# Kernel tuning notes

Hardware: AMD Instinct MI355X
Metric: run time of the kernel (lower is better)

## Reference

```python
import jax, jax.numpy as jnp
import numpy as np

B, L, D, H = 2, 2048, 1024, 16
HD = D // H
KW = 4  # conv kernel width


def layernorm(x, g, b, eps=1e-5):
    m = jnp.mean(x, axis=-1, keepdims=True)
    v = jnp.var(x, axis=-1, keepdims=True)
    return (x - m) / jnp.sqrt(v + eps) * g + b


def causal_conv(x, w, b):
    # torch Conv1d(k=4, padding=3, groups=D) then truncate to L => causal depthwise conv
    # out[t] = sum_j w[:, j] * x[t - 3 + j] + b
    xp = jnp.pad(x, ((0, 0), (KW - 1, 0), (0, 0)))
    Lx = x.shape[1]
    out = b
    for j in range(KW):
        out = out + xp[:, j:j + Lx, :] * w[:, j]
    return out


def setup_inputs() -> dict:
    key = jax.random.key(0)
    ks = jax.random.split(key, 16)
    r = lambda i, shape, s=0.02: jax.random.normal(ks[i], shape, jnp.float32) * s
    return dict(
        x=r(0, (B, L, D), 1.0),
        Wqkv=r(1, (D, 3 * D)), Wout=r(2, (D, D)),
        Wgate=r(3, (D, D)), bgate=jnp.zeros((D,), jnp.float32),
        fn_g=jnp.ones((D,), jnp.float32), fn_b=jnp.zeros((D,), jnp.float32),
        dn_g=jnp.ones((D,), jnp.float32), dn_b=jnp.zeros((D,), jnp.float32),
        dWq=r(4, (D, D)), dWk=r(5, (D, D)), dWv=r(6, (D, D)), dWo=r(7, (D, D)),
        Wbeta=r(8, (D, H)), bbeta=jnp.zeros((H,), jnp.float32),
        cq_w=r(9, (D, KW), 0.1), cq_b=jnp.zeros((D,), jnp.float32),
        ck_w=r(10, (D, KW), 0.1), ck_b=jnp.zeros((D,), jnp.float32),
        ln_g=jnp.ones((D,), jnp.float32), ln_b=jnp.zeros((D,), jnp.float32),
    )


def _delta_scan(q, k, v, beta):
    # q,k,v: (B,L,H,HD) ; beta: (B,L,H)
    Bx = q.shape[0]
    S0 = jnp.zeros((Bx, H, HD, HD), q.dtype)
    z0 = jnp.zeros((Bx, H, HD), q.dtype)

    def step(carry, inp):
        S, z = carry
        q_t, k_t, v_t, b_t = inp  # (B,H,HD) x3, (B,H)
        y = jnp.einsum('bhij,bhj->bhi', S, q_t)
        denom = jnp.einsum('bhi,bhi->bh', z, q_t)[..., None] + 1e-6
        y = y / denom
        old = jnp.einsum('bhij,bhj->bhi', S, k_t)
        delta = v_t - old
        S = S + b_t[..., None, None] * jnp.einsum('bhi,bhj->bhij', delta, k_t)
        z = z + b_t[..., None] * k_t
        return (S, z), y

    xs = (jnp.moveaxis(q, 1, 0), jnp.moveaxis(k, 1, 0),
          jnp.moveaxis(v, 1, 0), jnp.moveaxis(beta, 1, 0))
    (S, z), ys = jax.lax.scan(step, (S0, z0), xs)
    return jnp.moveaxis(ys, 0, 1), S, z  # (B,L,H,HD)


def _forward(x, Wqkv, Wout, Wgate, bgate, fn_g, fn_b, dn_g, dn_b,
             dWq, dWk, dWv, dWo, Wbeta, bbeta, cq_w, cq_b, ck_w, ck_b, ln_g, ln_b):
    Bx, Lx, Dx = x.shape
    # ---- flash (full causal, L<=2048 branch) ----
    qkv = (x @ Wqkv).reshape(Bx, Lx, 3, H, HD)
    q = jnp.moveaxis(qkv[:, :, 0], 1, 2)  # (B,H,L,HD)
    k = jnp.moveaxis(qkv[:, :, 1], 1, 2)
    v = jnp.moveaxis(qkv[:, :, 2], 1, 2)
    scale = HD ** -0.5
    scores = jnp.einsum('bhqd,bhkd->bhqk', q, k) * scale
    causal = jnp.tril(jnp.ones((Lx, Lx), bool))
    scores = jnp.where(causal, scores, -jnp.inf)
    attn = jax.nn.softmax(scores, axis=-1)
    flash = jnp.einsum('bhqk,bhkd->bhqd', attn, v)
    flash = jnp.moveaxis(flash, 1, 2).reshape(Bx, Lx, Dx) @ Wout
    flash = layernorm(flash, fn_g, fn_b)
    # ---- delta branch ----
    dq = causal_conv(x @ dWq, cq_w, cq_b).reshape(Bx, Lx, H, HD)
    dk = causal_conv(x @ dWk, ck_w, ck_b).reshape(Bx, Lx, H, HD)
    dv = (x @ dWv).reshape(Bx, Lx, H, HD)
    dk = dk / jnp.maximum(jnp.linalg.norm(dk, axis=-1, keepdims=True), 1e-12)
    beta = jax.nn.sigmoid(x @ Wbeta + bbeta)  # (B,L,H)
    ys, S, z = _delta_scan(dq, dk, dv, beta)
    delta_out = layernorm(ys.reshape(Bx, Lx, Dx) @ dWo, ln_g, ln_b)  # DeltaAttention layer_norm
    delta_out = layernorm(delta_out, dn_g, dn_b)  # hybrid delta_norm
    # ---- gate ----
    gate = jax.nn.sigmoid(x @ Wgate + bgate)
    out = gate * flash + (1.0 - gate) * delta_out
    return out, S, z


def reference(x, Wqkv, Wout, Wgate, bgate, fn_g, fn_b, dn_g, dn_b,
              dWq, dWk, dWv, dWo, Wbeta, bbeta, cq_w, cq_b, ck_w, ck_b, ln_g, ln_b):
    return _forward(x, Wqkv, Wout, Wgate, bgate, fn_g, fn_b, dn_g, dn_b,
                    dWq, dWk, dWv, dWo, Wbeta, bbeta, cq_w, cq_b, ck_w, ck_b, ln_g, ln_b)
```

## Files before the change

### kernel.cpp

```cpp
#include <hip/hip_runtime.h>
#include <hip/hip_bf16.h>

constexpr int B_ = 2, L_ = 2048, D_ = 1024, H_ = 16;

using bf16x8 = __attribute__((ext_vector_type(8))) short;
using f32x4  = __attribute__((ext_vector_type(4))) float;

__device__ __forceinline__ short f2b(float f) {
  union { float f; unsigned int u; } v; v.f = f;
  unsigned int r = (v.u + 0x7FFFu + ((v.u >> 16) & 1u)) >> 16;
  return (short)r;
}
__device__ __forceinline__ float b2f(unsigned short h) {
  union { unsigned int u; float f; } v; v.u = ((unsigned int)h) << 16; return v.f;
}
__device__ __forceinline__ void split2(float x, float y, unsigned int& h, unsigned int& l) {
  unsigned short hx = (unsigned short)f2b(x), hy = (unsigned short)f2b(y);
  h = (unsigned int)hx | ((unsigned int)hy << 16);
  unsigned short lx = (unsigned short)f2b(x - b2f(hx)), ly = (unsigned short)f2b(y - b2f(hy));
  l = (unsigned int)lx | ((unsigned int)ly << 16);
}
__device__ __forceinline__ float dot4(float4 a, float4 b) {
  return a.x * b.x + a.y * b.y + a.z * b.z + a.w * b.w;
}

__global__ __launch_bounds__(256) void tcast(const float* __restrict__ W, short* __restrict__ Wt,
                                             int N, int K) {
  __shared__ float T[64][65];
  int n0 = blockIdx.x * 64, k0 = blockIdx.y * 64;
  int tid = threadIdx.x;
#pragma unroll
  for (int i = 0; i < 16; ++i) {
    int idx = i * 256 + tid;
    int r = idx >> 6, c = idx & 63;
    T[r][c] = W[(size_t)(k0 + r) * N + n0 + c];
  }
  __syncthreads();
#pragma unroll
  for (int i = 0; i < 16; ++i) {
    int idx = i * 256 + tid;
    int rr = idx >> 6, cc = idx & 63;
    Wt[(size_t)(n0 + rr) * K + k0 + cc] = f2b(T[cc][rr]);
  }
}

__global__ __launch_bounds__(256) void tcast2(const float* __restrict__ W1, const float* __restrict__ W2,
                                              short* __restrict__ Wt1, short* __restrict__ Wt2) {
  __shared__ float T[64][65];
  const float* W = blockIdx.z ? W2 : W1;
  short* Wt = blockIdx.z ? Wt2 : Wt1;
  int n0 = blockIdx.x * 64, k0 = blockIdx.y * 64;
  int tid = threadIdx.x;
#pragma unroll
  for (int i = 0; i < 16; ++i) {
    int idx = i * 256 + tid;
    int r = idx >> 6, c = idx & 63;
    T[r][c] = W[(size_t)(k0 + r) * 1024 + n0 + c];
  }
  __syncthreads();
#pragma unroll
  for (int i = 0; i < 16; ++i) {
    int idx = i * 256 + tid;
    int rr = idx >> 6, cc = idx & 63;
    Wt[(size_t)(n0 + rr) * 1024 + k0 + cc] = f2b(T[cc][rr]);
  }
}

__global__ __launch_bounds__(256) void tcast_split2(const float* __restrict__ W1, const float* __restrict__ W2,
                                                    short* __restrict__ Wh1, short* __restrict__ Wl1,
                                                    short* __restrict__ Wh2, short* __restrict__ Wl2) {
  __shared__ float T[64][65];
  const float* W = blockIdx.z ? W2 : W1;
  short* Wh = blockIdx.z ? Wh2 : Wh1;
  short* Wl = blockIdx.z ? Wl2 : Wl1;
  int n0 = blockIdx.x * 64, k0 = blockIdx.y * 64;
  int tid = threadIdx.x;
#pragma unroll
  for (int i = 0; i < 16; ++i) {
    int idx = i * 256 + tid;
    int r = idx >> 6, c = idx & 63;
    T[r][c] = W[(size_t)(k0 + r) * 1024 + n0 + c];
  }
  __syncthreads();
#pragma unroll
  for (int i = 0; i < 16; ++i) {
    int idx = i * 256 + tid;
    int rr = idx >> 6, cc = idx & 63;
    float w = T[cc][rr];
    short h = f2b(w);
    short l = f2b(w - b2f((unsigned short)h));
    size_t o = (size_t)(n0 + rr) * 1024 + k0 + cc;
    Wh[o] = h;
    Wl[o] = l;
  }
}

template <int BN, typename CT>
__device__ __forceinline__ void gemm_bt_body(const float* __restrict__ A, const short* __restrict__ Wt,
                                             CT* __restrict__ C, int N, int K, int bx, int by) {
  constexpr int MT = (BN == 128) ? 4 : 2;
  constexpr int NT = 4;
  __shared__ __align__(16) short As[128 * 32];
  __shared__ __align__(16) short Bs[BN * 32];
  int tid = threadIdx.x;
  int wave = tid >> 6, lane = tid & 63, quad = lane >> 4, l15 = lane & 15;
  int m0 = by * 128, n0 = bx * BN;
  int wm = (BN == 128) ? (wave >> 1) * 64 : wave * 32;
  int wn = (BN == 128) ? (wave & 1) * 64 : 0;
  f32x4 acc[MT][NT];
#pragma unroll
  for (int mt = 0; mt < MT; ++mt)
#pragma unroll
    for (int nt = 0; nt < NT; ++nt) acc[mt][nt] = (f32x4){0.f, 0.f, 0.f, 0.f};

  for (int k0 = 0; k0 < K; k0 += 32) {
    __syncthreads();
#pragma unroll
    for (int i = 0; i < 2; ++i) {
      int chunk = i * 256 + tid;
      int m = chunk >> 2, kc = (chunk & 3) * 8;
      const float* ap = A + (size_t)(m0 + m) * K + k0 + kc;
      float4 a0 = *(const float4*)ap;
      float4 a1 = *(const float4*)(ap + 4);
      __hip_bfloat162 c0 = __float22bfloat162_rn(make_float2(a0.x, a0.y));
      __hip_bfloat162 c1 = __float22bfloat162_rn(make_float2(a0.z, a0.w));
      __hip_bfloat162 c2 = __float22bfloat162_rn(make_float2(a1.x, a1.y));
      __hip_bfloat162 c3 = __float22bfloat162_rn(make_float2(a1.z, a1.w));
      uint4 u;
      u.x = *(unsigned int*)&c0; u.y = *(unsigned int*)&c1;
      u.z = *(unsigned int*)&c2; u.w = *(unsigned int*)&c3;
      *(uint4*)&As[m * 32 + kc] = u;
    }
#pragma unroll
    for (int i = 0; i < BN * 4 / 256; ++i) {
      int chunk = i * 256 + tid;
      int n = chunk >> 2, kc = (chunk & 3) * 8;
      uint4 w = *(const uint4*)(Wt + (size_t)(n0 + n) * K + k0 + kc);
      *(uint4*)&Bs[n * 32 + kc] = w;
    }
    __syncthreads();
    bf16x8 af[MT], bf[NT];
#pragma unroll
    for (int mt = 0; mt < MT; ++mt) af[mt] = *(bf16x8*)&As[(wm + mt * 16 + l15) * 32 + quad * 8];
#pragma unroll
    for (int nt = 0; nt < NT; ++nt) bf[nt] = *(bf16x8*)&Bs[(wn + nt * 16 + l15) * 32 + quad * 8];
#pragma unroll
    for (int mt = 0; mt < MT; ++mt)
#pragma unroll
      for (int nt = 0; nt < NT; ++nt)
        acc[mt][nt] = __builtin_amdgcn_mfma_f32_16x16x32_bf16(af[mt], bf[nt], acc[mt][nt], 0, 0, 0);
  }
#pragma unroll
  for (int mt = 0; mt < MT; ++mt)
#pragma unroll
    for (int nt = 0; nt < NT; ++nt)
#pragma unroll
      for (int r = 0; r < 4; ++r) {
        size_t idx = (size_t)(m0 + wm + mt * 16 + quad * 4 + r) * N + n0 + wn + nt * 16 + l15;
        if constexpr (sizeof(CT) == 2) C[idx] = f2b(acc[mt][nt][r]);
        else C[idx] = acc[mt][nt][r];
      }
}

template <int BN>
__global__ __launch_bounds__(256) void gemm_bt(const float* __restrict__ A, const short* __restrict__ Wt,
                                               float* __restrict__ C, int N, int K) {
  gemm_bt_body<BN, float>(A, Wt, C, N, K, blockIdx.x, blockIdx.y);
}

__global__ __launch_bounds__(256) void gemm_bt_h(const float* __restrict__ A, const short* __restrict__ Wt,
                                                 short* __restrict__ C, int N, int K) {
  gemm_bt_body<128, short>(A, Wt, C, N, K, blockIdx.x, blockIdx.y);
}

__global__ __launch_bounds__(256) void gemm_bt2(const float* __restrict__ A, const short* __restrict__ Wt1,
                                                const short* __restrict__ Wt2, float* __restrict__ C1,
                                                float* __restrict__ C2) {
  gemm_bt_body<64, float>(A, blockIdx.z ? Wt2 : Wt1, blockIdx.z ? C2 : C1, 1024, 1024,
                          blockIdx.x, blockIdx.y);
}

__global__ __launch_bounds__(256) void gemm_bt_split2(const float* __restrict__ A,
                                                      const short* __restrict__ Wh1, const short* __restrict__ Wl1,
                                                      const short* __restrict__ Wh2, const short* __restrict__ Wl2,
                                                      float* __restrict__ C1, float* __restrict__ C2) {
  constexpr int K = 1024, N = 1024;
  const short* Wh = blockIdx.z ? Wh2 : Wh1;
  const short* Wl = blockIdx.z ? Wl2 : Wl1;
  float* C = blockIdx.z ? C2 : C1;
  __shared__ __align__(16) short Ash[128 * 32];
  __shared__ __align__(16) short Asl[128 * 32];
  __shared__ __align__(16) short Bsh[64 * 32];
  __shared__ __align__(16) short Bsl[64 * 32];
  int tid = threadIdx.x;
  int wave = tid >> 6, lane = tid & 63, quad = lane >> 4, l15 = lane & 15;
  int m0 = blockIdx.y * 128, n0 = blockIdx.x * 64;
  int wm = wave * 32;
  f32x4 acc[2][4];
#pragma unroll
  for (int mt = 0; mt < 2; ++mt)
#pragma unroll
    for (int nt = 0; nt < 4; ++nt) acc[mt][nt] = (f32x4){0.f, 0.f, 0.f, 0.f};

  for (int k0 = 0; k0 < K; k0 += 32) {
    __syncthreads();
#pragma unroll
    for (int i = 0; i < 2; ++i) {
      int chunk = i * 256 + tid;
      int m = chunk >> 2, kc = (chunk & 3) * 8;
      const float* ap = A + (size_t)(m0 + m) * K + k0 + kc;
      float4 a0 = *(const float4*)ap;
      float4 a1 = *(const float4*)(ap + 4);
      uint4 uh, ul;
      split2(a0.x, a0.y, uh.x, ul.x);
      split2(a0.z, a0.w, uh.y, ul.y);
      split2(a1.x, a1.y, uh.z, ul.z);
      split2(a1.z, a1.w, uh.w, ul.w);
      *(uint4*)&Ash[m * 32 + kc] = uh;
      *(uint4*)&Asl[m * 32 + kc] = ul;
    }
    {
      int n = tid >> 2, kc = (tid & 3) * 8;
      size_t off = (size_t)(n0 + n) * K + k0 + kc;
      *(uint4*)&Bsh[n * 32 + kc] = *(const uint4*)(Wh + off);
      *(uint4*)&Bsl[n * 32 + kc] = *(const uint4*)(Wl + off);
    }
    __syncthreads();
    bf16x8 ah[2], al[2], bh[4], bl[4];
#pragma unroll
    for (int mt = 0; mt < 2; ++mt) {
      ah[mt] = *(bf16x8*)&Ash[(wm + mt * 16 + l15) * 32 + quad * 8];
      al[mt] = *(bf16x8*)&Asl[(wm + mt * 16 + l15) * 32 + quad * 8];
    }
#pragma unroll
    for (int nt = 0; nt < 4; ++nt) {
      bh[nt] = *(bf16x8*)&Bsh[(nt * 16 + l15) * 32 + quad * 8];
      bl[nt] = *(bf16x8*)&Bsl[(nt * 16 + l15) * 32 + quad * 8];
    }
#pragma unroll
    for (int mt = 0; mt < 2; ++mt)
#pragma unroll
      for (int nt = 0; nt < 4; ++nt) {
        f32x4 a = acc[mt][nt];
        a = __builtin_amdgcn_mfma_f32_16x16x32_bf16(al[mt], bh[nt], a, 0, 0, 0);
        a = __builtin_amdgcn_mfma_f32_16x16x32_bf16(ah[mt], bl[nt], a, 0, 0, 0);
        a = __builtin_amdgcn_mfma_f32_16x16x32_bf16(ah[mt], bh[nt], a, 0, 0, 0);
        acc[mt][nt] = a;
      }
  }
#pragma unroll
  for (int mt = 0; mt < 2; ++mt)
#pragma unroll
    for (int nt = 0; nt < 4; ++nt)
#pragma unroll
      for (int r = 0; r < 4; ++r) {
        size_t idx = (size_t)(m0 + wm + mt * 16 + quad * 4 + r) * N + n0 + nt * 16 + l15;
        C[idx] = acc[mt][nt][r];
      }
}

__global__ __launch_bounds__(256) void attn_mfma(const short* __restrict__ qkv, float* __restrict__ outp) {
  __shared__ __align__(16) short Kl[64 * 64];
  __shared__ __align__(16) short Vt[64 * 64];
  __shared__ __align__(16) short Pl[64 * 64];
  int qb = 31 - blockIdx.x, h = blockIdx.y, b = blockIdx.z;
  int tid = threadIdx.x;
  int wave = tid >> 6, lane = tid & 63;
  int quad = lane >> 4, l15 = lane & 15;
  int qrow = qb * 64 + wave * 16 + l15;
  bf16x8 qf[2];
  {
    const short* qbase = qkv + (size_t)(b * L_ + qrow) * 3072 + h * 64;
#pragma unroll
    for (int s = 0; s < 2; ++s) qf[s] = *(const bf16x8*)(qbase + s * 32 + quad * 8);
  }
  f32x4 Of[4];
  float mrow[4], lrow[4], alpha[4];
#pragma unroll
  for (int dt = 0; dt < 4; ++dt) Of[dt] = (f32x4){0.f, 0.f, 0.f, 0.f};
#pragma unroll
  for (int r = 0; r < 4; ++r) { mrow[r] = -1e30f; lrow[r] = 0.f; }

  for (int kt = 0; kt <= qb; ++kt) {
    __syncthreads();
#pragma unroll
    for (int it = 0; it < 2; ++it) {
      int e8 = tid + it * 256;
      int key = e8 >> 3, g = e8 & 7;
      const short* src = qkv + ((size_t)((b * L_ + kt * 64 + key) * 3) + 1) * 1024 + h * 64 + g * 8;
      *(bf16x8*)&Kl[key * 64 + ((g ^ (key & 7)) << 3)] = *(const bf16x8*)src;
    }
    {
      int key4 = tid >> 4;
      int d4 = tid & 15;
      const short* vsrc = qkv + ((size_t)((b * L_ + kt * 64 + key4 * 4) * 3) + 2) * 1024 + h * 64 + d4 * 4;
      short4 v0 = *(const short4*)vsrc;
      short4 v1 = *(const short4*)(vsrc + 3072);
      short4 v2 = *(const short4*)(vsrc + 6144);
      short4 v3 = *(const short4*)(vsrc + 9216);
      short vr0[4] = {v0.x, v0.y, v0.z, v0.w};
      short vr1[4] = {v1.x, v1.y, v1.z, v1.w};
      short vr2[4] = {v2.x, v2.y, v2.z, v2.w};
      short vr3[4] = {v3.x, v3.y, v3.z, v3.w};
      int kg = key4 >> 1, k7b = (key4 & 1) * 4;
#pragma unroll
      for (int jj = 0; jj < 4; ++jj) {
        int d = d4 * 4 + jj;
        short4 sv;
        sv.x = vr0[jj]; sv.y = vr1[jj]; sv.z = vr2[jj]; sv.w = vr3[jj];
        *(short4*)&Vt[d * 64 + ((kg ^ (d & 7)) << 3) + k7b] = sv;
      }
    }
    __syncthreads();
    f32x4 sc[4];
#pragma unroll
    for (int nt = 0; nt < 4; ++nt) sc[nt] = (f32x4){0.f, 0.f, 0.f, 0.f};
#pragma unroll
    for (int s = 0; s < 2; ++s) {
#pragma unroll
      for (int nt = 0; nt < 4; ++nt) {
        int key = nt * 16 + l15;
        bf16x8 kf = *(bf16x8*)&Kl[key * 64 + (((4 * s + quad) ^ (key & 7)) << 3)];
        sc[nt] = __builtin_amdgcn_mfma_f32_16x16x32_bf16(qf[s], kf, sc[nt], 0, 0, 0);
      }
    }
    bool diag = (kt == qb);
#pragma unroll
    for (int r = 0; r < 4; ++r) {
      float sv[4];
#pragma unroll
      for (int nt = 0; nt < 4; ++nt) {
        float v = sc[nt][r] * 0.125f;
        if (diag && (nt * 16 + l15 > wave * 16 + quad * 4 + r)) v = -1e30f;
        sv[nt] = v;
      }
      float mx = fmaxf(fmaxf(sv[0], sv[1]), fmaxf(sv[2], sv[3]));
      mx = fmaxf(mx, __shfl_xor(mx, 1));
      mx = fmaxf(mx, __shfl_xor(mx, 2));
      mx = fmaxf(mx, __shfl_xor(mx, 4));
      mx = fmaxf(mx, __shfl_xor(mx, 8));
      float mnew = fmaxf(mrow[r], mx);
      float al = __expf(mrow[r] - mnew);
      mrow[r] = mnew;
      alpha[r] = al;
      int prow = wave * 16 + quad * 4 + r;
      int r7 = prow & 7;
      float ps = 0.f;
#pragma unroll
      for (int nt = 0; nt < 4; ++nt) {
        float p = __expf(sv[nt] - mnew);
        ps += p;
        Pl[prow * 64 + ((((nt << 1) + (l15 >> 3)) ^ r7) << 3) + (l15 & 7)] = f2b(p);
      }
      ps += __shfl_xor(ps, 1);
      ps += __shfl_xor(ps, 2);
      ps += __shfl_xor(ps, 4);
      ps += __shfl_xor(ps, 8);
      lrow[r] = lrow[r] * al + ps;
    }
#pragma unroll
    for (int dt = 0; dt < 4; ++dt)
#pragma unroll
      for (int r = 0; r < 4; ++r) Of[dt][r] *= alpha[r];
#pragma unroll
    for (int s = 0; s < 2; ++s) {
      bf16x8 pf = *(bf16x8*)&Pl[(wave * 16 + l15) * 64 + (((4 * s + quad) ^ (l15 & 7)) << 3)];
#pragma unroll
      for (int dt = 0; dt < 4; ++dt) {
        int d = dt * 16 + l15;
        bf16x8 vf = *(bf16x8*)&Vt[d * 64 + (((4 * s + quad) ^ (d & 7)) << 3)];
        Of[dt] = __builtin_amdgcn_mfma_f32_16x16x32_bf16(pf, vf, Of[dt], 0, 0, 0);
      }
    }
  }
#pragma unroll
  for (int r = 0; r < 4; ++r) alpha[r] = 1.f / lrow[r];
  int orow = qb * 64 + wave * 16 + quad * 4;
#pragma unroll
  for (int dt = 0; dt < 4; ++dt)
#pragma unroll
    for (int r = 0; r < 4; ++r)
      outp[(size_t)(b * L_ + orow + r) * 1024 + h * 64 + dt * 16 + l15] = Of[dt][r] * alpha[r];
}

__global__ __launch_bounds__(256) void ln_kernel(float* __restrict__ X, const float* __restrict__ g,
                                                 const float* __restrict__ bb) {
  int row = blockIdx.x, tid = threadIdx.x;
  float* xr = X + (size_t)row * D_;
  float v[4], s = 0.f, ss = 0.f;
#pragma unroll
  for (int i = 0; i < 4; ++i) { v[i] = xr[tid + i * 256]; s += v[i]; ss += v[i] * v[i]; }
#pragma unroll
  for (int off = 32; off; off >>= 1) { s += __shfl_xor(s, off); ss += __shfl_xor(ss, off); }
  __shared__ float rs[4], rss[4];
  if ((tid & 63) == 0) { rs[tid >> 6] = s; rss[tid >> 6] = ss; }
  __syncthreads();
  float S = rs[0] + rs[1] + rs[2] + rs[3];
  float SS = rss[0] + rss[1] + rss[2] + rss[3];
  float mean = S * (1.f / 1024.f);
  float var = SS * (1.f / 1024.f) - mean * mean;
  float inv = rsqrtf(var + 1e-5f);
#pragma unroll
  for (int i = 0; i < 4; ++i) {
    int c = tid + i * 256;
    xr[c] = (v[i] - mean) * inv * g[c] + bb[c];
  }
}

__global__ __launch_bounds__(256) void ln2mix_kernel(const float* __restrict__ X,
                                                     const float* __restrict__ g1, const float* __restrict__ b1,
                                                     const float* __restrict__ g2, const float* __restrict__ b2,
                                                     const float* __restrict__ gpre, const float* __restrict__ bgate,
                                                     const float* __restrict__ fo, float* __restrict__ outp) {
  int row = blockIdx.x, tid = threadIdx.x;
  const float* xr = X + (size_t)row * D_;
  __shared__ float rs[4], rss[4];
  float v[4], s = 0.f, ss = 0.f;
#pragma unroll
  for (int i = 0; i < 4; ++i) { v[i] = xr[tid + i * 256]; s += v[i]; ss += v[i] * v[i]; }
#pragma unroll
  for (int off = 32; off; off >>= 1) { s += __shfl_xor(s, off); ss += __shfl_xor(ss, off); }
  if ((tid & 63) == 0) { rs[tid >> 6] = s; rss[tid >> 6] = ss; }
  __syncthreads();
  float S = rs[0] + rs[1] + rs[2] + rs[3];
  float SS = rss[0] + rss[1] + rss[2] + rss[3];
  float mean = S * (1.f / 1024.f);
  float var = SS * (1.f / 1024.f) - mean * mean;
  float inv = rsqrtf(var + 1e-5f);
  s = 0.f; ss = 0.f;
#pragma unroll
  for (int i = 0; i < 4; ++i) {
    int c = tid + i * 256;
    v[i] = (v[i] - mean) * inv * g1[c] + b1[c];
    s += v[i]; ss += v[i] * v[i];
  }
#pragma unroll
  for (int off = 32; off; off >>= 1) { s += __shfl_xor(s, off); ss += __shfl_xor(ss, off); }
  __syncthreads();
  if ((tid & 63) == 0) { rs[tid >> 6] = s; rss[tid >> 6] = ss; }
  __syncthreads();
  S = rs[0] + rs[1] + rs[2] + rs[3];
  SS = rss[0] + rss[1] + rss[2] + rss[3];
  mean = S * (1.f / 1024.f);
  var = SS * (1.f / 1024.f) - mean * mean;
  inv = rsqrtf(var + 1e-5f);
#pragma unroll
  for (int i = 0; i < 4; ++i) {
    int c = tid + i * 256;
    size_t idx = (size_t)row * D_ + c;
    float w = (v[i] - mean) * inv * g2[c] + b2[c];
    float gg = 1.f / (1.f + __expf(-(gpre[idx] + bgate[c])));
    outp[idx] = gg * fo[idx] + (1.f - gg) * w;
  }
}

__global__ __launch_bounds__(256) void convnorm_kernel(const float* __restrict__ qin, const float* __restrict__ kin,
                                                       const float* __restrict__ qw, const float* __restrict__ qb,
                                                       const float* __restrict__ kw, const float* __restrict__ kb,
                                                       float* __restrict__ qout, float* __restrict__ kout) {
  int path = blockIdx.y;
  int row = blockIdx.x * 4 + (threadIdx.x >> 6);
  int lane = threadIdx.x & 63;
  int bl = row >> 4, h = row & 15;
  int t = bl & (L_ - 1);
  int d = h * 64 + lane;
  size_t idx = (size_t)bl * D_ + d;
  const float* xin = path ? kin : qin;
  const float* w = path ? kw : qw;
  const float* bias = path ? kb : qb;
  float acc = bias[d];
#pragma unroll
  for (int j = 0; j < 4; ++j) {
    int tt = t - 3 + j;
    if (tt >= 0) acc += w[d * 4 + j] * xin[idx + (size_t)(j - 3) * D_];
  }
  if (path) {
    float n2 = acc * acc;
#pragma unroll
    for (int off = 32; off; off >>= 1) n2 += __shfl_xor(n2, off);
    acc = acc / fmaxf(sqrtf(n2), 1e-12f);
    kout[idx] = acc;
  } else {
    qout[idx] = acc;
  }
}

__global__ __launch_bounds__(256) void beta_kernel(const float* __restrict__ xf, const float* __restrict__ Wb,
                                                   const float* __restrict__ bb, float* __restrict__ beta) {
  int row = blockIdx.x, tid = threadIdx.x;
  int h = tid & 15, seg = tid >> 4;
  const float* xr = xf + (size_t)row * D_ + seg * 64;
  const float* wp = Wb + (seg * 64) * H_ + h;
  float p = 0.f;
  for (int k = 0; k < 64; ++k) p += xr[k] * wp[k * H_];
  __shared__ float red[16][17];
  red[seg][h] = p;
  __syncthreads();
  if (tid < 16) {
    float s = bb[tid];
#pragma unroll
    for (int s2 = 0; s2 < 16; ++s2) s += red[s2][tid];
    beta[(size_t)row * H_ + tid] = 1.f / (1.f + __expf(-s));
  }
}

__global__ __launch_bounds__(256) void prep_kernel(const float* __restrict__ dq, const float* __restrict__ dk,
                                                   const float* __restrict__ beta,
                                                   float* __restrict__ Minv_g, float* __restrict__ Bq_g) {
  __shared__ __align__(16) float Kl[32 * 68];
  __shared__ __align__(16) float Ql[32 * 68];
  __shared__ __align__(16) float Ml[32 * 36];
  __shared__ __align__(16) float Xl[32 * 36];
  __shared__ __align__(16) float bl[32];
  int c = blockIdx.x, bh = blockIdx.y;
  int b = bh >> 4, h = bh & 15;
  int t0 = c * 32;
  int tid = threadIdx.x;
#pragma unroll
  for (int rep = 0; rep < 2; ++rep) {
    int id = tid * 2 + rep;
    int r = id >> 4, j4 = id & 15;
    size_t gi = (size_t)(b * L_ + t0 + r) * 1024 + h * 64 + j4 * 4;
    *(float4*)&Kl[r * 68 + j4 * 4] = *(const float4*)&dk[gi];
    *(float4*)&Ql[r * 68 + j4 * 4] = *(const float4*)&dq[gi];
  }
  if (tid < 32) bl[tid] = beta[(size_t)(b * L_ + t0 + tid) * 16 + h];
  __syncthreads();
  int t = tid >> 3, s0 = (tid & 7) * 4;
  float accA[4] = {0.f, 0.f, 0.f, 0.f}, accB[4] = {0.f, 0.f, 0.f, 0.f};
#pragma unroll
  for (int k4 = 0; k4 < 16; ++k4) {
    float4 kt = *(float4*)&Kl[t * 68 + k4 * 4];
    float4 qt = *(float4*)&Ql[t * 68 + k4 * 4];
#pragma unroll
    for (int j = 0; j < 4; ++j) {
      float4 ks = *(float4*)&Kl[(s0 + j) * 68 + k4 * 4];
      accA[j] += dot4(kt, ks);
      accB[j] += dot4(qt, ks);
    }
  }
  float4 bq;
  float* bqp = (float*)&bq;
#pragma unroll
  for (int j = 0; j < 4; ++j) {
    int s = s0 + j;
    Ml[t * 36 + s] = (s < t) ? bl[t] * accA[j] : ((s == t) ? 1.f : 0.f);
    bqp[j] = (s < t) ? accB[j] : 0.f;
  }
  size_t obase = ((size_t)(bh * 64 + c) * 32 + t) * 32 + s0;
  *(float4*)&Bq_g[obase] = bq;
  __syncthreads();
  if (tid < 32) {
    int col = tid;
    float xr[32];
#pragma unroll
    for (int tt = 0; tt < 32; ++tt) {
      float x = (tt == col) ? 1.f : 0.f;
#pragma unroll
      for (int s = 0; s < tt; ++s) x -= Ml[tt * 36 + s] * xr[s];
      xr[tt] = x;
      Xl[tt * 36 + col] = x;
    }
  }
  __syncthreads();
  float4 mv = make_float4(Xl[t * 36 + s0], Xl[t * 36 + s0 + 1], Xl[t * 36 + s0 + 2], Xl[t * 36 + s0 + 3]);
  *(float4*)&Minv_g[obase] = mv;
}

__global__ __launch_bounds__(256) void delta_kernel(const float* __restrict__ dq, const float* __restrict__ dk,
                                                    const float* __restrict__ dv, const float* __restrict__ beta,
                                                    const float* __restrict__ Minv_g, const float* __restrict__ Bq_g,
                                                    float* __restrict__ ys, float* __restrict__ outS,
                                                    float* __restrict__ outZ) {
  __shared__ __align__(16) float Kl[32 * 68];
  __shared__ __align__(16) float Ql[32 * 68];
  __shared__ __align__(16) float Vl[32 * 5];
  __shared__ __align__(16) float Mil[32 * 36];
  __shared__ __align__(16) float Bql[32 * 36];
  __shared__ __align__(16) float bl[32];
  __shared__ __align__(16) float S0l[4 * 68];
  __shared__ __align__(16) float Y0l[32 * 5];
  __shared__ __align__(16) float RtmpTl[4 * 36];
  __shared__ __align__(16) float RTl[4 * 36];
  __shared__ __align__(16) float z0l[68];
  __shared__ __align__(16) float qzl[32];
  __shared__ __align__(16) float denl[32];
  int bh = blockIdx.x & 31, grp = blockIdx.x >> 5;
  int b = bh >> 4, h = bh & 15;
  int i0 = grp * 4;
  int tid = threadIdx.x;
  int r = tid >> 3, j8 = (tid & 7) * 8, s4 = tid & 7;
  size_t kqbase = (size_t)(b * L_) * 1024 + h * 64;

  for (int e = tid; e < 4 * 68; e += 256) S0l[e] = 0.f;
  if (tid < 68) z0l[tid] = 0.f;

  float4 kA, kB, qA, qB, mr, br;
  float vr = 0.f, blr = 0.f;
  {
    const float* kp = dk + kqbase + (size_t)r * 1024 + j8;
    kA = ((const float4*)kp)[0]; kB = ((const float4*)kp)[1];
    const float* qp = dq + kqbase + (size_t)r * 1024 + j8;
    qA = ((const float4*)qp)[0]; qB = ((const float4*)qp)[1];
    size_t gb = ((size_t)(bh * 64) * 32 + r) * 32 + s4 * 4;
    mr = *(const float4*)&Minv_g[gb];
    br = *(const float4*)&Bq_g[gb];
    if (tid < 128) vr = dv[(size_t)(b * L_ + (tid >> 2)) * 1024 + h * 64 + i0 + (tid & 3)];
    if (tid < 32) blr = beta[(size_t)(b * L_ + tid) * 16 + h];
  }
  *(float4*)&Kl[r * 68 + j8] = kA; *(float4*)&Kl[r * 68 + j8 + 4] = kB;
  *(float4*)&Ql[r * 68 + j8] = qA; *(float4*)&Ql[r * 68 + j8 + 4] = qB;
  *(float4*)&Mil[r * 36 + s4 * 4] = mr;
  *(float4*)&Bql[r * 36 + s4 * 4] = br;
  if (tid < 128) Vl[(tid >> 2) * 5 + (tid & 3)] = vr;
  if (tid < 32) bl[tid] = blr;
  __syncthreads();

  for (int c = 0; c < 64; ++c) {
    int cn = (c + 1 < 64) ? c + 1 : 63;
    int t0n = cn * 32;
    {
      const float* kp = dk + kqbase + (size_t)(t0n + r) * 1024 + j8;
      kA = ((const float4*)kp)[0]; kB = ((const float4*)kp)[1];
      const float* qp = dq + kqbase + (size_t)(t0n + r) * 1024 + j8;
      qA = ((const float4*)qp)[0]; qB = ((const float4*)qp)[1];
      size_t gb = ((size_t)(bh * 64 + cn) * 32 + r) * 32 + s4 * 4;
      mr = *(const float4*)&Minv_g[gb];
      br = *(const float4*)&Bq_g[gb];
      if (tid < 128) vr = dv[(size_t)(b * L_ + t0n + (tid >> 2)) * 1024 + h * 64 + i0 + (tid & 3)];
      if (tid < 32) blr = beta[(size_t)(b * L_ + t0n + tid) * 16 + h];
    }
    int t0 = c * 32;
    {
      int jh = tid & 1;
      int i = (tid >> 1) & 3;
      int t = tid >> 3;
      float aK = 0.f, aY = 0.f;
#pragma unroll
      for (int jj = 0; jj < 8; ++jj) {
        int j4 = jh * 8 + jj;
        float4 k = *(float4*)&Kl[t * 68 + j4 * 4];
        float4 q = *(float4*)&Ql[t * 68 + j4 * 4];
        float4 s = *(float4*)&S0l[i * 68 + j4 * 4];
        aK += dot4(k, s);
        aY += dot4(q, s);
      }
      aK += __shfl_xor(aK, 1);
      aY += __shfl_xor(aY, 1);
      if (jh == 0) {
        float be = bl[t];
        RtmpTl[i * 36 + t] = be * (Vl[t * 5 + i] - aK);
        Y0l[t * 5 + i] = aY;
      }
      if (tid < 32) {
        float a = 0.f;
#pragma unroll
        for (int j4 = 0; j4 < 16; ++j4) {
          float4 q = *(float4*)&Ql[tid * 68 + j4 * 4];
          float4 z = *(float4*)&z0l[j4 * 4];
          a += dot4(q, z);
        }
        qzl[tid] = a;
      }
    }
    __syncthreads();
    {
      if (tid < 128) {
        int t = tid >> 2, i = tid & 3;
        float acc = 0.f;
#pragma unroll
        for (int s4i = 0; s4i < 8; ++s4i) {
          float4 m = *(float4*)&Mil[t * 36 + s4i * 4];
          float4 rt = *(float4*)&RtmpTl[i * 36 + s4i * 4];
          acc += dot4(m, rt);
        }
        RTl[i * 36 + t] = acc;
      } else if (tid < 160) {
        int t = tid - 128;
        float a = qzl[t];
#pragma unroll
        for (int s4i = 0; s4i < 8; ++s4i) {
          float4 bq = *(float4*)&Bql[t * 36 + s4i * 4];
          float4 be = *(float4*)&bl[s4i * 4];
          a += dot4(bq, be);
        }
        denl[t] = a + 1e-6f;
      }
    }
    __syncthreads();
    if (tid < 128) {
      int t = tid >> 2, i = tid & 3;
      float acc = 0.f;
#pragma unroll
      for (int s4i = 0; s4i < 8; ++s4i) {
        float4 bq = *(float4*)&Bql[t * 36 + s4i * 4];
        float4 rt = *(float4*)&RTl[i * 36 + s4i * 4];
        acc += dot4(bq, rt);
      }
      float y = (Y0l[t * 5 + i] + acc) / denl[t];
      ys[(size_t)(b * L_ + t0 + t) * 1024 + h * 64 + i0 + i] = y;
    }
    {
      int i = tid >> 6, j = tid & 63;
      float a = S0l[i * 68 + j];
#pragma unroll
      for (int s4i = 0; s4i < 8; ++s4i) {
        float4 rt = *(float4*)&RTl[i * 36 + s4i * 4];
        a += rt.x * Kl[(s4i * 4 + 0) * 68 + j]
           + rt.y * Kl[(s4i * 4 + 1) * 68 + j]
           + rt.z * Kl[(s4i * 4 + 2) * 68 + j]
           + rt.w * Kl[(s4i * 4 + 3) * 68 + j];
      }
      S0l[i * 68 + j] = a;
    }
    if (tid >= 128 && tid < 192) {
      int j = tid - 128;
      float a = z0l[j];
#pragma unroll
      for (int s = 0; s < 32; ++s) a += bl[s] * Kl[s * 68 + j];
      z0l[j] = a;
    }
    __syncthreads();
    *(float4*)&Kl[r * 68 + j8] = kA; *(float4*)&Kl[r * 68 + j8 + 4] = kB;
    *(float4*)&Ql[r * 68 + j8] = qA; *(float4*)&Ql[r * 68 + j8 + 4] = qB;
    *(float4*)&Mil[r * 36 + s4 * 4] = mr;
    *(float4*)&Bql[r * 36 + s4 * 4] = br;
    if (tid < 128) Vl[(tid >> 2) * 5 + (tid & 3)] = vr;
    if (tid < 32) bl[tid] = blr;
    __syncthreads();
  }
  {
    int i = tid >> 6, j = tid & 63;
    outS[((size_t)(bh * 64) + i0 + i) * 64 + j] = S0l[i * 68 + j];
  }
  if (grp == 0 && tid < 64) outZ[bh * 64 + tid] = z0l[tid];
}

extern "C" void kernel_launch(void* const* d_in, const int* in_sizes, int n_in,
                              void* d_out, int out_size, void* d_ws, size_t ws_size,
                              hipStream_t stream) {
  const float* x     = (const float*)d_in[0];
  const float* Wqkv  = (const float*)d_in[1];
  const float* Wout  = (const float*)d_in[2];
  const float* Wgate = (const float*)d_in[3];
  const float* bgate = (const float*)d_in[4];
  const float* fn_g  = (const float*)d_in[5];
  const float* fn_b  = (const float*)d_in[6];
  const float* dn_g  = (const float*)d_in[7];
  const float* dn_b  = (const float*)d_in[8];
  const float* dWq   = (const float*)d_in[9];
  const float* dWk   = (const float*)d_in[10];
  const float* dWv   = (const float*)d_in[11];
  const float* dWo   = (const float*)d_in[12];
  const float* Wbeta = (const float*)d_in[13];
  const float* bbeta = (const float*)d_in[14];
  const float* cq_w  = (const float*)d_in[15];
  const float* cq_b  = (const float*)d_in[16];
  const float* ck_w  = (const float*)d_in[17];
  const float* ck_b  = (const float*)d_in[18];
  const float* ln_g  = (const float*)d_in[19];
  const float* ln_b  = (const float*)d_in[20];

  float* ws = (float*)d_ws;
  short* qkvh   = (short*)ws;
  float* dv     = ws;
  float* dqc    = ws + 4194304;
  float* dkc    = ws + 8388608;
  float* attnO  = ws + 12582912;
  short* wtg    = (short*)(ws + 12582912);
  short* Wvt    = (short*)(ws + 14680064);
  float* Minv_g = ws + 12582912;
  float* Bq_g   = ws + 14680064;
  float* do1    = ws + 12582912;
  float* fo     = ws + 16777216;
  float* dqp    = ws + 20971520;
  float* gpre   = ws + 20971520;
  float* dkp    = ws + 25165824;
  float* ysb    = ws + 25165824;
  float* betab  = ws + 29360128;

  short* Wqkvt = (short*)(ws + 20971520);
  short* Woutt = (short*)(ws + 29426688);
  short* Wot   = (short*)(ws + 4194304);

  short* Wqh = (short*)(ws + 8388608);
  short* Wql = (short*)(ws + 8912896);
  short* Wkh = (short*)(ws + 9437184);
  short* Wkl = (short*)(ws + 9961472);

  float* out  = (float*)d_out;
  float* outS = out + 4194304;
  float* outZ = out + 4325376;

  tcast<<<dim3(48, 16), 256, 0, stream>>>(Wqkv, Wqkvt, 3072, 1024);
  gemm_bt_h<<<dim3(24, 32), 256, 0, stream>>>(x, Wqkvt, qkvh, 3072, 1024);
  attn_mfma<<<dim3(32, H_, B_), 256, 0, stream>>>(qkvh, attnO);
  tcast<<<dim3(16, 16), 256, 0, stream>>>(Wout, Woutt, 1024, 1024);
  gemm_bt<64><<<dim3(16, 32), 256, 0, stream>>>(attnO, Woutt, fo, 1024, 1024);
  ln_kernel<<<4096, 256, 0, stream>>>(fo, fn_g, fn_b);
  tcast_split2<<<dim3(16, 16, 2), 256, 0, stream>>>(dWq, dWk, Wqh, Wql, Wkh, Wkl);
  gemm_bt_split2<<<dim3(16, 32, 2), 256, 0, stream>>>(x, Wqh, Wql, Wkh, Wkl, dqp, dkp);
  convnorm_kernel<<<dim3(16384, 2), 256, 0, stream>>>(dqp, dkp, cq_w, cq_b, ck_w, ck_b, dqc, dkc);
  beta_kernel<<<4096, 256, 0, stream>>>(x, Wbeta, bbeta, betab);
  tcast2<<<dim3(16, 16, 2), 256, 0, stream>>>(dWv, Wgate, Wvt, wtg);
  gemm_bt2<<<dim3(16, 32, 2), 256, 0, stream>>>(x, Wvt, wtg, dv, gpre);
  prep_kernel<<<dim3(64, 32), 256, 0, stream>>>(dqc, dkc, betab, Minv_g, Bq_g);
  delta_kernel<<<512, 256, 0, stream>>>(dqc, dkc, dv, betab, Minv_g, Bq_g, ysb, outS, outZ);
  tcast<<<dim3(16, 16), 256, 0, stream>>>(dWo, Wot, 1024, 1024);
  gemm_bt<64><<<dim3(16, 32), 256, 0, stream>>>(ysb, Wot, do1, 1024, 1024);
  ln2mix_kernel<<<4096, 256, 0, stream>>>(do1, ln_g, ln_b, dn_g, dn_b, gpre, bgate, fo, out);
}
```

Baseline: 778.2 us.

## Precompute Minv-folded chunk matrices in prep and double-buffer delta scan

The prep kernel now folds the triangular inverse into Minv·K and Bq·Minv, and also precomputes the denominator correction and the z increment for each chunk. This removes one dependent matmul stage and one barrier from the serial delta loop. The delta loop double-buffers its shared-memory chunk data so the end-of-iteration store and barrier pair collapses into one. ys is staged in the output buffer to free workspace, at the cost of more prep work and more shared memory.

```diff
diff --git a/kernel.cpp b/kernel.cpp
--- a/kernel.cpp
+++ b/kernel.cpp
@@ -506,11 +506,13 @@
 
 __global__ __launch_bounds__(256) void prep_kernel(const float* __restrict__ dq, const float* __restrict__ dk,
                                                    const float* __restrict__ beta,
-                                                   float* __restrict__ Minv_g, float* __restrict__ Bq_g) {
+                                                   float* __restrict__ MK_g, float* __restrict__ BqM_g,
+                                                   float* __restrict__ denB_g, float* __restrict__ zinc_g) {
   __shared__ __align__(16) float Kl[32 * 68];
   __shared__ __align__(16) float Ql[32 * 68];
   __shared__ __align__(16) float Ml[32 * 36];
   __shared__ __align__(16) float Xl[32 * 36];
+  __shared__ __align__(16) float Bql[32 * 36];
   __shared__ __align__(16) float bl[32];
   int c = blockIdx.x, bh = blockIdx.y;
   int b = bh >> 4, h = bh & 15;
@@ -539,16 +541,12 @@
       accB[j] += dot4(qt, ks);
     }
   }
-  float4 bq;
-  float* bqp = (float*)&bq;
 #pragma unroll
   for (int j = 0; j < 4; ++j) {
     int s = s0 + j;
     Ml[t * 36 + s] = (s < t) ? bl[t] * accA[j] : ((s == t) ? 1.f : 0.f);
-    bqp[j] = (s < t) ? accB[j] : 0.f;
-  }
-  size_t obase = ((size_t)(bh * 64 + c) * 32 + t) * 32 + s0;
-  *(float4*)&Bq_g[obase] = bq;
+    Bql[t * 36 + s] = (s < t) ? accB[j] : 0.f;
+  }
   __syncthreads();
   if (tid < 32) {
     int col = tid;
@@ -563,172 +561,179 @@
     }
   }
   __syncthreads();
-  float4 mv = make_float4(Xl[t * 36 + s0], Xl[t * 36 + s0 + 1], Xl[t * 36 + s0 + 2], Xl[t * 36 + s0 + 3]);
-  *(float4*)&Minv_g[obase] = mv;
+  size_t cb = (size_t)(bh * 64 + c);
+  {
+    int s = tid >> 3, j8 = (tid & 7) * 8;
+    float4 m0 = make_float4(0.f, 0.f, 0.f, 0.f);
+    float4 m1 = make_float4(0.f, 0.f, 0.f, 0.f);
+#pragma unroll
+    for (int t2 = 0; t2 < 32; ++t2) {
+      float xv = Xl[t2 * 36 + s];
+      float4 k0 = *(float4*)&Kl[t2 * 68 + j8];
+      float4 k1 = *(float4*)&Kl[t2 * 68 + j8 + 4];
+      m0.x += xv * k0.x; m0.y += xv * k0.y; m0.z += xv * k0.z; m0.w += xv * k0.w;
+      m1.x += xv * k1.x; m1.y += xv * k1.y; m1.z += xv * k1.z; m1.w += xv * k1.w;
+    }
+    float* mkp = MK_g + (cb * 32 + s) * 64 + j8;
+    *(float4*)mkp = m0;
+    *(float4*)(mkp + 4) = m1;
+  }
+  {
+    int tt = tid >> 3, s4 = (tid & 7) * 4;
+    float4 acc = make_float4(0.f, 0.f, 0.f, 0.f);
+#pragma unroll
+    for (int u4 = 0; u4 < 8; ++u4) {
+      float4 bq = *(float4*)&Bql[tt * 36 + u4 * 4];
+      float4 x0 = *(float4*)&Xl[(u4 * 4 + 0) * 36 + s4];
+      float4 x1 = *(float4*)&Xl[(u4 * 4 + 1) * 36 + s4];
+      float4 x2 = *(float4*)&Xl[(u4 * 4 + 2) * 36 + s4];
+      float4 x3 = *(float4*)&Xl[(u4 * 4 + 3) * 36 + s4];
+      acc.x += bq.x * x0.x + bq.y * x1.x + bq.z * x2.x + bq.w * x3.x;
+      acc.y += bq.x * x0.y + bq.y * x1.y + bq.z * x2.y + bq.w * x3.y;
+      acc.z += bq.x * x0.z + bq.y * x1.z + bq.z * x2.z + bq.w * x3.z;
+      acc.w += bq.x * x0.w + bq.y * x1.w + bq.z * x2.w + bq.w * x3.w;
+    }
+    *(float4*)&BqM_g[cb * 1024 + tt * 32 + s4] = acc;
+  }
+  if (tid < 32) {
+    float a = 0.f;
+#pragma unroll
+    for (int s4i = 0; s4i < 8; ++s4i)
+      a += dot4(*(float4*)&Bql[tid * 36 + s4i * 4], *(float4*)&bl[s4i * 4]);
+    denB_g[cb * 32 + tid] = a;
+  }
+  if (tid >= 64 && tid < 128) {
+    int j = tid - 64;
+    float a = 0.f;
+#pragma unroll
+    for (int s = 0; s < 32; ++s) a += bl[s] * Kl[s * 68 + j];
+    zinc_g[cb * 64 + j] = a;
+  }
 }
 
 __global__ __launch_bounds__(256) void delta_kernel(const float* __restrict__ dq, const float* __restrict__ dk,
                                                     const float* __restrict__ dv, const float* __restrict__ beta,
-                                                    const float* __restrict__ Minv_g, const float* __restrict__ Bq_g,
+                                                    const float* __restrict__ MK_g, const float* __restrict__ BqM_g,
+                                                    const float* __restrict__ denB_g, const float* __restrict__ zinc_g,
                                                     float* __restrict__ ys, float* __restrict__ outS,
                                                     float* __restrict__ outZ) {
-  __shared__ __align__(16) float Kl[32 * 68];
-  __shared__ __align__(16) float Ql[32 * 68];
-  __shared__ __align__(16) float Vl[32 * 5];
-  __shared__ __align__(16) float Mil[32 * 36];
-  __shared__ __align__(16) float Bql[32 * 36];
-  __shared__ __align__(16) float bl[32];
+  __shared__ __align__(16) float Kl[2][32 * 68];
+  __shared__ __align__(16) float Ql[2][32 * 68];
+  __shared__ __align__(16) float MKl[2][32 * 68];
+  __shared__ __align__(16) float BqMl[2][32 * 36];
+  __shared__ __align__(16) float Vl[2][32 * 5];
+  __shared__ __align__(16) float bll[2][32];
+  __shared__ __align__(16) float dnl[2][32];
+  __shared__ __align__(16) float zil[2][64];
   __shared__ __align__(16) float S0l[4 * 68];
   __shared__ __align__(16) float Y0l[32 * 5];
-  __shared__ __align__(16) float RtmpTl[4 * 36];
-  __shared__ __align__(16) float RTl[4 * 36];
-  __shared__ __align__(16) float z0l[68];
+  __shared__ __align__(16) float Rtl[4 * 36];
+  __shared__ __align__(16) float z0l[64];
   __shared__ __align__(16) float qzl[32];
-  __shared__ __align__(16) float denl[32];
   int bh = blockIdx.x & 31, grp = blockIdx.x >> 5;
   int b = bh >> 4, h = bh & 15;
   int i0 = grp * 4;
   int tid = threadIdx.x;
-  int r = tid >> 3, j8 = (tid & 7) * 8, s4 = tid & 7;
+  int r = tid >> 3, j8 = (tid & 7) * 8;
   size_t kqbase = (size_t)(b * L_) * 1024 + h * 64;
 
   for (int e = tid; e < 4 * 68; e += 256) S0l[e] = 0.f;
-  if (tid < 68) z0l[tid] = 0.f;
-
-  float4 kA, kB, qA, qB, mr, br;
-  float vr = 0.f, blr = 0.f;
-  {
-    const float* kp = dk + kqbase + (size_t)r * 1024 + j8;
-    kA = ((const float4*)kp)[0]; kB = ((const float4*)kp)[1];
-    const float* qp = dq + kqbase + (size_t)r * 1024 + j8;
-    qA = ((const float4*)qp)[0]; qB = ((const float4*)qp)[1];
-    size_t gb = ((size_t)(bh * 64) * 32 + r) * 32 + s4 * 4;
-    mr = *(const float4*)&Minv_g[gb];
-    br = *(const float4*)&Bq_g[gb];
-    if (tid < 128) vr = dv[(size_t)(b * L_ + (tid >> 2)) * 1024 + h * 64 + i0 + (tid & 3)];
-    if (tid < 32) blr = beta[(size_t)(b * L_ + tid) * 16 + h];
-  }
-  *(float4*)&Kl[r * 68 + j8] = kA; *(float4*)&Kl[r * 68 + j8 + 4] = kB;
-  *(float4*)&Ql[r * 68 + j8] = qA; *(float4*)&Ql[r * 68 + j8 + 4] = qB;
-  *(float4*)&Mil[r * 36 + s4 * 4] = mr;
-  *(float4*)&Bql[r * 36 + s4 * 4] = br;
-  if (tid < 128) Vl[(tid >> 2) * 5 + (tid & 3)] = vr;
-  if (tid < 32) bl[tid] = blr;
+  if (tid < 64) z0l[tid] = 0.f;
+
+  float4 kA, kB, qA, qB, mA, mB, bqA, bqB;
+  bqA = bqB = make_float4(0.f, 0.f, 0.f, 0.f);
+  float vr = 0.f, blr = 0.f, dnb = 0.f, zi = 0.f;
+
+#define DLOAD(CN) { \
+    size_t rb_ = kqbase + (size_t)((CN) * 32 + r) * 1024 + j8; \
+    kA = ((const float4*)(dk + rb_))[0]; kB = ((const float4*)(dk + rb_))[1]; \
+    qA = ((const float4*)(dq + rb_))[0]; qB = ((const float4*)(dq + rb_))[1]; \
+    size_t cb_ = (size_t)(bh * 64 + (CN)); \
+    const float* mkp_ = MK_g + (cb_ * 32 + r) * 64 + j8; \
+    mA = ((const float4*)mkp_)[0]; mB = ((const float4*)mkp_)[1]; \
+    if (tid < 128) { \
+      const float* bqp_ = BqM_g + cb_ * 1024 + (tid >> 2) * 32 + (tid & 3) * 8; \
+      bqA = ((const float4*)bqp_)[0]; bqB = ((const float4*)bqp_)[1]; \
+      vr = dv[(size_t)(b * L_ + (CN) * 32 + (tid >> 2)) * 1024 + h * 64 + i0 + (tid & 3)]; \
+    } \
+    if (tid < 32) { blr = beta[(size_t)(b * L_ + (CN) * 32 + tid) * 16 + h]; dnb = denB_g[cb_ * 32 + tid]; } \
+    if (tid < 64) zi = zinc_g[cb_ * 64 + tid]; \
+  }
+#define DSTORE(NX) { \
+    *(float4*)&Kl[NX][r * 68 + j8] = kA; *(float4*)&Kl[NX][r * 68 + j8 + 4] = kB; \
+    *(float4*)&Ql[NX][r * 68 + j8] = qA; *(float4*)&Ql[NX][r * 68 + j8 + 4] = qB; \
+    *(float4*)&MKl[NX][r * 68 + j8] = mA; *(float4*)&MKl[NX][r * 68 + j8 + 4] = mB; \
+    if (tid < 128) { \
+      int t_ = tid >> 2, s8_ = (tid & 3) * 8; \
+      *(float4*)&BqMl[NX][t_ * 36 + s8_] = bqA; \
+      *(float4*)&BqMl[NX][t_ * 36 + s8_ + 4] = bqB; \
+      Vl[NX][t_ * 5 + (tid & 3)] = vr; \
+    } \
+    if (tid < 32) { bll[NX][tid] = blr; dnl[NX][tid] = dnb; } \
+    if (tid < 64) zil[NX][tid] = zi; \
+  }
+
+  DLOAD(0);
+  DSTORE(0);
   __syncthreads();
 
   for (int c = 0; c < 64; ++c) {
+    int cur = c & 1, nxt = cur ^ 1;
     int cn = (c + 1 < 64) ? c + 1 : 63;
-    int t0n = cn * 32;
-    {
-      const float* kp = dk + kqbase + (size_t)(t0n + r) * 1024 + j8;
-      kA = ((const float4*)kp)[0]; kB = ((const float4*)kp)[1];
-      const float* qp = dq + kqbase + (size_t)(t0n + r) * 1024 + j8;
-      qA = ((const float4*)qp)[0]; qB = ((const float4*)qp)[1];
-      size_t gb = ((size_t)(bh * 64 + cn) * 32 + r) * 32 + s4 * 4;
-      mr = *(const float4*)&Minv_g[gb];
-      br = *(const float4*)&Bq_g[gb];
-      if (tid < 128) vr = dv[(size_t)(b * L_ + t0n + (tid >> 2)) * 1024 + h * 64 + i0 + (tid & 3)];
-      if (tid < 32) blr = beta[(size_t)(b * L_ + t0n + tid) * 16 + h];
-    }
-    int t0 = c * 32;
-    {
-      int jh = tid & 1;
-      int i = (tid >> 1) & 3;
-      int t = tid >> 3;
-      float aK = 0.f, aY = 0.f;
-#pragma unroll
-      for (int jj = 0; jj < 8; ++jj) {
-        int j4 = jh * 8 + jj;
-        float4 k = *(float4*)&Kl[t * 68 + j4 * 4];
-        float4 q = *(float4*)&Ql[t * 68 + j4 * 4];
-        float4 s = *(float4*)&S0l[i * 68 + j4 * 4];
-        aK += dot4(k, s);
-        aY += dot4(q, s);
-      }
-      aK += __shfl_xor(aK, 1);
-      aY += __shfl_xor(aY, 1);
-      if (jh == 0) {
-        float be = bl[t];
-        RtmpTl[i * 36 + t] = be * (Vl[t * 5 + i] - aK);
-        Y0l[t * 5 + i] = aY;
-      }
-      if (tid < 32) {
-        float a = 0.f;
-#pragma unroll
-        for (int j4 = 0; j4 < 16; ++j4) {
-          float4 q = *(float4*)&Ql[tid * 68 + j4 * 4];
-          float4 z = *(float4*)&z0l[j4 * 4];
-          a += dot4(q, z);
-        }
-        qzl[tid] = a;
-      }
+    DLOAD(cn);
+    if (tid < 128) {
+      int s = tid >> 2, i = tid & 3;
+      float aK = 0.f;
+#pragma unroll
+      for (int j4 = 0; j4 < 16; ++j4)
+        aK += dot4(*(float4*)&Kl[cur][s * 68 + j4 * 4], *(float4*)&S0l[i * 68 + j4 * 4]);
+      Rtl[i * 36 + s] = bll[cur][s] * (Vl[cur][s * 5 + i] - aK);
+    } else {
+      int t = (tid >> 2) & 31, i = tid & 3;
+      float aY = 0.f;
+#pragma unroll
+      for (int j4 = 0; j4 < 16; ++j4)
+        aY += dot4(*(float4*)&Ql[cur][t * 68 + j4 * 4], *(float4*)&S0l[i * 68 + j4 * 4]);
+      Y0l[t * 5 + i] = aY;
+    }
+    if (tid < 32) {
+      float a = 0.f;
+#pragma unroll
+      for (int j4 = 0; j4 < 16; ++j4)
+        a += dot4(*(float4*)&Ql[cur][tid * 68 + j4 * 4], *(float4*)&z0l[j4 * 4]);
+      qzl[tid] = a;
     }
     __syncthreads();
     {
-      if (tid < 128) {
-        int t = tid >> 2, i = tid & 3;
-        float acc = 0.f;
-#pragma unroll
-        for (int s4i = 0; s4i < 8; ++s4i) {
-          float4 m = *(float4*)&Mil[t * 36 + s4i * 4];
-          float4 rt = *(float4*)&RtmpTl[i * 36 + s4i * 4];
-          acc += dot4(m, rt);
-        }
-        RTl[i * 36 + t] = acc;
-      } else if (tid < 160) {
-        int t = tid - 128;
-        float a = qzl[t];
-#pragma unroll
-        for (int s4i = 0; s4i < 8; ++s4i) {
-          float4 bq = *(float4*)&Bql[t * 36 + s4i * 4];
-          float4 be = *(float4*)&bl[s4i * 4];
-          a += dot4(bq, be);
-        }
-        denl[t] = a + 1e-6f;
+      int i2 = tid >> 6, j = tid & 63;
+      float a = S0l[i2 * 68 + j];
+#pragma unroll
+      for (int s4i = 0; s4i < 8; ++s4i) {
+        float4 rt = *(float4*)&Rtl[i2 * 36 + s4i * 4];
+        a += rt.x * MKl[cur][(s4i * 4 + 0) * 68 + j]
+           + rt.y * MKl[cur][(s4i * 4 + 1) * 68 + j]
+           + rt.z * MKl[cur][(s4i * 4 + 2) * 68 + j]
+           + rt.w * MKl[cur][(s4i * 4 + 3) * 68 + j];
       }
-    }
-    __syncthreads();
+      S0l[i2 * 68 + j] = a;
+    }
     if (tid < 128) {
       int t = tid >> 2, i = tid & 3;
-      float acc = 0.f;
-#pragma unroll
-      for (int s4i = 0; s4i < 8; ++s4i) {
-        float4 bq = *(float4*)&Bql[t * 36 + s4i * 4];
-        float4 rt = *(float4*)&RTl[i * 36 + s4i * 4];
-        acc += dot4(bq, rt);
-      }
-      float y = (Y0l[t * 5 + i] + acc) / denl[t];
-      ys[(size_t)(b * L_ + t0 + t) * 1024 + h * 64 + i0 + i] = y;
-    }
-    {
-      int i = tid >> 6, j = tid & 63;
-      float a = S0l[i * 68 + j];
-#pragma unroll
-      for (int s4i = 0; s4i < 8; ++s4i) {
-        float4 rt = *(float4*)&RTl[i * 36 + s4i * 4];
-        a += rt.x * Kl[(s4i * 4 + 0) * 68 + j]
-           + rt.y * Kl[(s4i * 4 + 1) * 68 + j]
-           + rt.z * Kl[(s4i * 4 + 2) * 68 + j]
-           + rt.w * Kl[(s4i * 4 + 3) * 68 + j];
-      }
-      S0l[i * 68 + j] = a;
-    }
-    if (tid >= 128 && tid < 192) {
+      float acc = Y0l[t * 5 + i];
+#pragma unroll
+      for (int s4i = 0; s4i < 8; ++s4i)
+        acc += dot4(*(float4*)&BqMl[cur][t * 36 + s4i * 4], *(float4*)&Rtl[i * 36 + s4i * 4]);
+      float y = acc / (qzl[t] + dnl[cur][t] + 1e-6f);
+      ys[(size_t)(b * L_ + c * 32 + t) * 1024 + h * 64 + i0 + i] = y;
+    } else if (tid < 192) {
       int j = tid - 128;
-      float a = z0l[j];
-#pragma unroll
-      for (int s = 0; s < 32; ++s) a += bl[s] * Kl[s * 68 + j];
-      z0l[j] = a;
-    }
+      z0l[j] += zil[cur][j];
+    }
+    DSTORE(nxt);
     __syncthreads();
-    *(float4*)&Kl[r * 68 + j8] = kA; *(float4*)&Kl[r * 68 + j8 + 4] = kB;
-    *(float4*)&Ql[r * 68 + j8] = qA; *(float4*)&Ql[r * 68 + j8 + 4] = qB;
-    *(float4*)&Mil[r * 36 + s4 * 4] = mr;
-    *(float4*)&Bql[r * 36 + s4 * 4] = br;
-    if (tid < 128) Vl[(tid >> 2) * 5 + (tid & 3)] = vr;
-    if (tid < 32) bl[tid] = blr;
-    __syncthreads();
-  }
+  }
+#undef DLOAD
+#undef DSTORE
   {
     int i = tid >> 6, j = tid & 63;
     outS[((size_t)(bh * 64) + i0 + i) * 64 + j] = S0l[i * 68 + j];
@@ -769,14 +774,15 @@
   float* attnO  = ws + 12582912;
   short* wtg    = (short*)(ws + 12582912);
   short* Wvt    = (short*)(ws + 14680064);
-  float* Minv_g = ws + 12582912;
-  float* Bq_g   = ws + 14680064;
+  float* denB_g = ws + 12582912;
+  float* zinc_g = ws + 12582912 + 65536;
+  float* BqM_g  = ws + 14680064;
   float* do1    = ws + 12582912;
   float* fo     = ws + 16777216;
   float* dqp    = ws + 20971520;
   float* gpre   = ws + 20971520;
   float* dkp    = ws + 25165824;
-  float* ysb    = ws + 25165824;
+  float* MK_g   = ws + 25165824;
   float* betab  = ws + 29360128;
 
   short* Wqkvt = (short*)(ws + 20971520);
@@ -791,6 +797,7 @@
   float* out  = (float*)d_out;
   float* outS = out + 4194304;
   float* outZ = out + 4325376;
+  float* ysb  = out;
 
   tcast<<<dim3(48, 16), 256, 0, stream>>>(Wqkv, Wqkvt, 3072, 1024);
   gemm_bt_h<<<dim3(24, 32), 256, 0, stream>>>(x, Wqkvt, qkvh, 3072, 1024);
@@ -804,8 +811,8 @@
   beta_kernel<<<4096, 256, 0, stream>>>(x, Wbeta, bbeta, betab);
   tcast2<<<dim3(16, 16, 2), 256, 0, stream>>>(dWv, Wgate, Wvt, wtg);
   gemm_bt2<<<dim3(16, 32, 2), 256, 0, stream>>>(x, Wvt, wtg, dv, gpre);
-  prep_kernel<<<dim3(64, 32), 256, 0, stream>>>(dqc, dkc, betab, Minv_g, Bq_g);
-  delta_kernel<<<512, 256, 0, stream>>>(dqc, dkc, dv, betab, Minv_g, Bq_g, ysb, outS, outZ);
+  prep_kernel<<<dim3(64, 32), 256, 0, stream>>>(dqc, dkc, betab, MK_g, BqM_g, denB_g, zinc_g);
+  delta_kernel<<<512, 256, 0, stream>>>(dqc, dkc, dv, betab, MK_g, BqM_g, denB_g, zinc_g, ysb, outS, outZ);
   tcast<<<dim3(16, 16), 256, 0, stream>>>(dWo, Wot, 1024, 1024);
   gemm_bt<64><<<dim3(16, 32), 256, 0, stream>>>(ysb, Wot, do1, 1024, 1024);
   ln2mix_kernel<<<4096, 256, 0, stream>>>(do1, ln_g, ln_b, dn_g, dn_b, gpre, bgate, fo, out);
```

After: 791.1 us. Within noise of the previous version (+1.7%).
